# Performance work log

Hardware: AMD Instinct MI355X
Metric: run time of the kernel (lower is better)

## Reference

```python
import jax, jax.numpy as jnp
import numpy as np

B, T, N, K, IB, O = 128, 16, 65536, 8, 256, 10

def setup_inputs() -> dict:
    key = jax.random.key(0)
    ks = jax.random.split(key, 8)
    x = jax.random.randint(ks[0], (B, T, IB), 0, 2, dtype=jnp.int32)          # boolean input bits per timestep
    adj_list = jax.random.randint(ks[1], (N, K), 0, N, dtype=jnp.int32)       # incoming neighbors, homogenized
    adj_mask = jnp.ones((N, K), dtype=jnp.int32)                               # validity mask (all valid here)
    lut = jax.random.randint(ks[2], (N, 2 ** K), 0, 2, dtype=jnp.int32)        # boolean lookup table per node
    init_state = jax.random.randint(ks[3], (N,), 0, 2, dtype=jnp.int32)        # 'random' init strategy
    w_in = jnp.arange(IB, dtype=jnp.int32)                                     # input-bit -> node index map
    w_readout = jax.random.normal(ks[4], (O, N), dtype=jnp.float32) * 0.01
    b_readout = jax.random.normal(ks[5], (O,), dtype=jnp.float32)
    return dict(x=x, adj_list=adj_list, adj_mask=adj_mask, lut=lut,
                init_state=init_state, w_in=w_in,
                w_readout=w_readout, b_readout=b_readout)

def _run_reservoir(x, adj_list, adj_mask, lut, init_state, w_in):
    # x: [B,T,IB] bits; returns final boolean state [B,N] (int32)
    powers = (2 ** jnp.arange(K, dtype=jnp.int32))[::-1]   # matches powers_of_2 flip
    node_idx = jnp.arange(N, dtype=jnp.int32)
    state0 = jnp.broadcast_to(init_state[None, :], (B, N)).astype(jnp.int32)

    def step(state, xt):
        # perturb input nodes with this timestep's bits (xor perturbation)
        state = state.at[:, w_in].set(jnp.bitwise_xor(state[:, w_in], xt))
        # gather incoming-neighbor states, mask padded slots: [B,N,K]
        neigh = jnp.take(state, adj_list, axis=1) * adj_mask
        # pack K bits into LUT index, MSB-first: [B,N]
        idx = jnp.sum(neigh * powers, axis=-1)
        # per-node boolean update via LUT gather
        new_state = lut[node_idx[None, :], idx]
        return new_state, None

    xT = jnp.swapaxes(x, 0, 1)  # [T,B,IB]
    final, _ = jax.lax.scan(step, state0, xT)
    return final

def reference(x, adj_list, adj_mask, lut, init_state, w_in, w_readout, b_readout):
    final = _run_reservoir(x, adj_list, adj_mask, lut, init_state, w_in)
    logits = final.astype(jnp.float32) @ w_readout.T + b_readout  # [B,O]
    return jax.nn.sigmoid(logits)
```

## Files before the change

kernel.cpp:

```cpp
#include <hip/hip_runtime.h>
#include <stdint.h>

#define NN     65536
#define KK     8
#define BB     128
#define TT     16
#define IBITS  256
#define OO     10

#define ZIDX         (NN + IBITS)
#define SBUF_ENTRIES (NN + IBITS + 1)
#define RCHUNKS 512
#define RNODES  128

__device__ __forceinline__ uint32_t bmask(uint32_t w, int off) {
  return (uint32_t)__builtin_amdgcn_sbfe((int)w, off, 1);
}
__device__ __forceinline__ uint32_t mux(uint32_t s, uint32_t hi, uint32_t lo) {
  return ((hi ^ lo) & s) ^ lo;
}

template<int D, int BASE> struct Sh {
  static __device__ __forceinline__ void eval(const uint32_t (&L)[8],
      const uint32_t (&xa)[8], const uint32_t (&xb)[8],
      uint32_t &ra, uint32_t &rb) {
    uint32_t la, lb, ha, hb;
    Sh<D - 1, BASE>::eval(L, xa, xb, la, lb);
    Sh<D - 1, BASE + (1 << (D - 1))>::eval(L, xa, xb, ha, hb);
    ra = mux(xa[D - 1], ha, la);
    rb = mux(xb[D - 1], hb, lb);
  }
};
template<int BASE> struct Sh<2, BASE> {
  static __device__ __forceinline__ void eval(const uint32_t (&L)[8],
      const uint32_t (&xa)[8], const uint32_t (&xb)[8],
      uint32_t &ra, uint32_t &rb) {
    const uint32_t lw = L[BASE >> 5];
    const uint32_t c0 = bmask(lw, (BASE & 31) + 0);
    const uint32_t c1 = bmask(lw, (BASE & 31) + 1);
    const uint32_t c2 = bmask(lw, (BASE & 31) + 2);
    const uint32_t c3 = bmask(lw, (BASE & 31) + 3);
    uint32_t t0, t1;
    t0 = mux(xa[0], c1, c0); t1 = mux(xa[0], c3, c2); ra = mux(xa[1], t1, t0);
    t0 = mux(xb[0], c1, c0); t1 = mux(xb[0], c3, c2); rb = mux(xb[1], t1, t0);
  }
};

#define PB_LUT   2048
#define PB_MADJ  2048
#define PB_X     64
#define PB_STATE 256
#define PREP_BLOCKS (PB_LUT + PB_MADJ + PB_X + PB_STATE)

__global__ __launch_bounds__(256) void prep_kernel(
    const int* __restrict__ lut, const int* __restrict__ adj,
    const int* __restrict__ adjm, const int* __restrict__ x,
    const int* __restrict__ init,
    uint32_t* __restrict__ luttt, int* __restrict__ madj,
    uint32_t* __restrict__ xvecw, uint4* __restrict__ sA, uint4* __restrict__ sB) {
  const int b = blockIdx.x, t = threadIdx.x;
  if (b < PB_LUT) {
    const int g = b * 256 + t;
    const int n = g >> 3, w = g & 7;
    const int4* lut4 = (const int4*)lut;
    uint32_t val = 0;
#pragma unroll
    for (int q = 0; q < 8; ++q) {
      int4 v = lut4[n * 64 + w * 8 + q];
      val |= (uint32_t)(v.x & 1) << (4 * q + 0);
      val |= (uint32_t)(v.y & 1) << (4 * q + 1);
      val |= (uint32_t)(v.z & 1) << (4 * q + 2);
      val |= (uint32_t)(v.w & 1) << (4 * q + 3);
    }
    luttt[g] = val;
  } else if (b < PB_LUT + PB_MADJ) {
    const int g = (b - PB_LUT) * 256 + t;
    int a = adj[g];
    int m = adjm[g] & 1;
    madj[g] = m ? ((a < IBITS) ? a + NN : a) : ZIDX;
  } else if (b < PB_LUT + PB_MADJ + PB_X) {
    const int g = (b - PB_LUT - PB_MADJ) * 256 + t;
    const int tt = g >> 10, rest = g & 1023, i = rest >> 2, bq = rest & 3;
    uint32_t wv = 0;
#pragma unroll
    for (int bl = 0; bl < 32; ++bl) {
      int bb = bq * 32 + bl;
      wv |= (uint32_t)(x[(bb * TT + tt) * IBITS + i] & 1) << bl;
    }
    xvecw[(tt * IBITS + i) * 4 + bq] = wv;
  } else {
    const int n = (b - PB_LUT - PB_MADJ - PB_X) * 256 + t;
    uint32_t m = 0u - (uint32_t)(init[n] & 1);
    uint4 s = make_uint4(m, m, m, m);
    sA[n] = s;
    if (n < IBITS) {
      uint32_t wv[4] = {0, 0, 0, 0};
#pragma unroll
      for (int bb = 0; bb < BB; ++bb) {
        uint32_t bit = (uint32_t)(x[(bb * TT + 0) * IBITS + n] & 1);
        wv[bb >> 5] |= bit << (bb & 31);
      }
      sA[NN + n] = make_uint4(s.x ^ wv[0], s.y ^ wv[1], s.z ^ wv[2], s.w ^ wv[3]);
    }
    if (n == 0) {
      uint4 z = make_uint4(0, 0, 0, 0);
      sA[ZIDX] = z;
      sB[ZIDX] = z;
    }
  }
}

__global__ __launch_bounds__(256) void step_kernel(const uint32_t* __restrict__ sinw,
                                                   uint32_t* __restrict__ soutw,
                                                   const uint4* __restrict__ luttt,
                                                   const int* __restrict__ madj,
                                                   const uint32_t* __restrict__ xnextw) {
  const int g = blockIdx.x * 256 + threadIdx.x;
  const int n = g >> 1, h = g & 1;
  const int4* madj4 = (const int4*)madj;
  int4 a0 = madj4[n * 2 + 0], a1 = madj4[n * 2 + 1];
  uint4 l0 = luttt[n * 2 + 0], l1 = luttt[n * 2 + 1];
  const int ia[8] = {a0.x, a0.y, a0.z, a0.w, a1.x, a1.y, a1.z, a1.w};
  uint32_t xa[8], xb[8];
#pragma unroll
  for (int k = 0; k < 8; ++k) {
    uint2 gg = *(const uint2*)(sinw + (ia[k] << 2) + (h << 1));
    xa[7 - k] = gg.x;
    xb[7 - k] = gg.y;
  }
  const uint32_t L[8] = {l0.x, l0.y, l0.z, l0.w, l1.x, l1.y, l1.z, l1.w};
  uint32_t ra, rb;
  Sh<8, 0>::eval(L, xa, xb, ra, rb);
  *(uint2*)(soutw + (n << 2) + (h << 1)) = make_uint2(ra, rb);
  if (xnextw != nullptr && n < IBITS) {
    uint2 xn = *(const uint2*)(xnextw + (n << 2) + (h << 1));
    *(uint2*)(soutw + ((NN + n) << 2) + (h << 1)) = make_uint2(ra ^ xn.x, rb ^ xn.y);
  }
}

__global__ __launch_bounds__(256) void readout_kernel(const uint32_t* __restrict__ statew,
                                                      const float* __restrict__ w,
                                                      float* __restrict__ part) {
  __shared__ uint32_t sw[64 * 4];
  __shared__ float wsm[OO * 64];
  const int c = blockIdx.x;
  const int t = threadIdx.x;
  const int b = t & 127, oh = t >> 7;
  const int word = b >> 5, sh = b & 31;
  float acc[5] = {0.f, 0.f, 0.f, 0.f, 0.f};
  for (int s = 0; s < 2; ++s) {
    const int base = c * RNODES + s * 64;
    __syncthreads();
    sw[t] = statew[base * 4 + t];
#pragma unroll
    for (int r = 0; r < 3; ++r) {
      int idx = r * 256 + t;
      if (idx < OO * 64) wsm[idx] = w[(idx >> 6) * NN + base + (idx & 63)];
    }
    __syncthreads();
#pragma unroll 8
    for (int j = 0; j < 64; ++j) {
      uint32_t m = 0u - ((sw[j * 4 + word] >> sh) & 1u);
#pragma unroll
      for (int q = 0; q < 5; ++q) {
        uint32_t wv = __float_as_uint(wsm[(oh * 5 + q) * 64 + j]) & m;
        acc[q] += __uint_as_float(wv);
      }
    }
  }
#pragma unroll
  for (int q = 0; q < 5; ++q)
    part[(c * BB + b) * OO + oh * 5 + q] = acc[q];
}

__global__ __launch_bounds__(256) void finalize_kernel(const float* __restrict__ part,
                                                       const float* __restrict__ bias,
                                                       float* __restrict__ out) {
  __shared__ float red[256];
  const int i = blockIdx.x;
  const int b = i / OO, o = i % OO;
  const int t = threadIdx.x;
  float s = part[(t * BB + b) * OO + o] + part[((t + 256) * BB + b) * OO + o];
  red[t] = s;
  __syncthreads();
  for (int h = 128; h > 0; h >>= 1) {
    if (t < h) red[t] += red[t + h];
    __syncthreads();
  }
  if (t == 0) out[b * OO + o] = 1.f / (1.f + __expf(-(red[0] + bias[o])));
}

extern "C" void kernel_launch(void* const* d_in, const int* in_sizes, int n_in,
                              void* d_out, int out_size, void* d_ws, size_t ws_size,
                              hipStream_t stream) {
  const int* x    = (const int*)d_in[0];
  const int* adj  = (const int*)d_in[1];
  const int* adjm = (const int*)d_in[2];
  const int* lut  = (const int*)d_in[3];
  const int* init = (const int*)d_in[4];
  const float* wro = (const float*)d_in[6];
  const float* bro = (const float*)d_in[7];
  float* out = (float*)d_out;

  char* ws = (char*)d_ws;
  const size_t SBUF = (size_t)SBUF_ENTRIES * 16;
  uint4* sA        = (uint4*)(ws);
  uint4* sB        = (uint4*)(ws + SBUF);
  uint32_t* xvecw  = (uint32_t*)(ws + 2 * SBUF);
  uint32_t* luttt  = (uint32_t*)(ws + 2 * SBUF + (size_t)TT * IBITS * 16);
  int* madj        = (int*)(ws + 2 * SBUF + (size_t)TT * IBITS * 16 + (size_t)NN * 32);
  float* part      = (float*)(ws + 2 * SBUF + (size_t)TT * IBITS * 16 + (size_t)NN * 64);

  hipLaunchKernelGGL(prep_kernel, dim3(PREP_BLOCKS), dim3(256), 0, stream,
                     lut, adj, adjm, x, init, luttt, madj, xvecw, sA, sB);

  for (int t = 0; t < TT; ++t) {
    const uint32_t* sin = (const uint32_t*)((t & 1) ? sB : sA);
    uint32_t* sout      = (uint32_t*)((t & 1) ? sA : sB);
    const uint32_t* xn  = (t + 1 < TT) ? (xvecw + (size_t)(t + 1) * IBITS * 4) : nullptr;
    hipLaunchKernelGGL(step_kernel, dim3((NN * 2) / 256), dim3(256), 0, stream,
                       sin, sout, (const uint4*)luttt, madj, xn);
  }
  hipLaunchKernelGGL(readout_kernel, dim3(RCHUNKS), dim3(256), 0, stream,
                     (const uint32_t*)sA, wro, part);
  hipLaunchKernelGGL(finalize_kernel, dim3(BB * OO), dim3(256), 0, stream, part, bro, out);
}
```

Before: 296.0 us.

## Fuse all timesteps into one persistent kernel with a software grid barrier

Replaces the sixteen per-timestep step kernel launches with one persistent kernel of 1024 blocks. The blocks synchronize between timesteps through a striped atomic-counter grid barrier, and each thread keeps its LUT and neighbor offsets in registers across all steps. Each thread now handles one 32-batch word per node instead of two, and the counters are zeroed in the prep kernel. This removes launch gaps and the repeated reloading of LUT and adjacency data. In exchange it relies on all 1024 blocks being co-resident; otherwise the barrier deadlocks, and the barrier itself adds latency at every step.

```diff
diff --git a/kernel.cpp b/kernel.cpp
--- a/kernel.cpp
+++ b/kernel.cpp
@@ -12,6 +12,7 @@
 #define SBUF_ENTRIES (NN + IBITS + 1)
 #define RCHUNKS 512
 #define RNODES  128
+#define SP_BLOCKS 1024
 
 __device__ __forceinline__ uint32_t bmask(uint32_t w, int off) {
   return (uint32_t)__builtin_amdgcn_sbfe((int)w, off, 1);
@@ -20,29 +21,25 @@
   return ((hi ^ lo) & s) ^ lo;
 }
 
-template<int D, int BASE> struct Sh {
-  static __device__ __forceinline__ void eval(const uint32_t (&L)[8],
-      const uint32_t (&xa)[8], const uint32_t (&xb)[8],
-      uint32_t &ra, uint32_t &rb) {
-    uint32_t la, lb, ha, hb;
-    Sh<D - 1, BASE>::eval(L, xa, xb, la, lb);
-    Sh<D - 1, BASE + (1 << (D - 1))>::eval(L, xa, xb, ha, hb);
-    ra = mux(xa[D - 1], ha, la);
-    rb = mux(xb[D - 1], hb, lb);
+template<int D, int BASE> struct Sh1 {
+  static __device__ __forceinline__ uint32_t eval(const uint32_t (&L)[8],
+                                                  const uint32_t (&xv)[8]) {
+    uint32_t lo = Sh1<D - 1, BASE>::eval(L, xv);
+    uint32_t hi = Sh1<D - 1, BASE + (1 << (D - 1))>::eval(L, xv);
+    return mux(xv[D - 1], hi, lo);
   }
 };
-template<int BASE> struct Sh<2, BASE> {
-  static __device__ __forceinline__ void eval(const uint32_t (&L)[8],
-      const uint32_t (&xa)[8], const uint32_t (&xb)[8],
-      uint32_t &ra, uint32_t &rb) {
+template<int BASE> struct Sh1<2, BASE> {
+  static __device__ __forceinline__ uint32_t eval(const uint32_t (&L)[8],
+                                                  const uint32_t (&xv)[8]) {
     const uint32_t lw = L[BASE >> 5];
     const uint32_t c0 = bmask(lw, (BASE & 31) + 0);
     const uint32_t c1 = bmask(lw, (BASE & 31) + 1);
     const uint32_t c2 = bmask(lw, (BASE & 31) + 2);
     const uint32_t c3 = bmask(lw, (BASE & 31) + 3);
-    uint32_t t0, t1;
-    t0 = mux(xa[0], c1, c0); t1 = mux(xa[0], c3, c2); ra = mux(xa[1], t1, t0);
-    t0 = mux(xb[0], c1, c0); t1 = mux(xb[0], c3, c2); rb = mux(xb[1], t1, t0);
+    const uint32_t t0 = mux(xv[0], c1, c0);
+    const uint32_t t1 = mux(xv[0], c3, c2);
+    return mux(xv[1], t1, t0);
   }
 };
 
@@ -57,7 +54,8 @@
     const int* __restrict__ adjm, const int* __restrict__ x,
     const int* __restrict__ init,
     uint32_t* __restrict__ luttt, int* __restrict__ madj,
-    uint32_t* __restrict__ xvecw, uint4* __restrict__ sA, uint4* __restrict__ sB) {
+    uint32_t* __restrict__ xvecw, uint4* __restrict__ sA, uint4* __restrict__ sB,
+    uint32_t* __restrict__ ctrs) {
   const int b = blockIdx.x, t = threadIdx.x;
   if (b < PB_LUT) {
     const int g = b * 256 + t;
@@ -102,6 +100,7 @@
       }
       sA[NN + n] = make_uint4(s.x ^ wv[0], s.y ^ wv[1], s.z ^ wv[2], s.w ^ wv[3]);
     }
+    if (n < 512) ctrs[n] = 0;
     if (n == 0) {
       uint4 z = make_uint4(0, 0, 0, 0);
       sA[ZIDX] = z;
@@ -110,31 +109,58 @@
   }
 }
 
-__global__ __launch_bounds__(256) void step_kernel(const uint32_t* __restrict__ sinw,
-                                                   uint32_t* __restrict__ soutw,
-                                                   const uint4* __restrict__ luttt,
-                                                   const int* __restrict__ madj,
-                                                   const uint32_t* __restrict__ xnextw) {
+__device__ __forceinline__ void grid_barrier(uint32_t* ctrs, uint32_t phase) {
+  __syncthreads();
+  if (threadIdx.x == 0) {
+    __threadfence();
+    atomicAdd(&ctrs[(blockIdx.x & 31) * 16], 1u);
+  }
+  if (threadIdx.x < 32) {
+    const uint32_t tgt = phase * (SP_BLOCKS / 32);
+    while (__hip_atomic_load(&ctrs[threadIdx.x * 16], __ATOMIC_RELAXED,
+                             __HIP_MEMORY_SCOPE_AGENT) < tgt) {
+      __builtin_amdgcn_s_sleep(2);
+    }
+  }
+  __syncthreads();
+  if (threadIdx.x < 64) __threadfence();
+  __syncthreads();
+}
+
+__global__ __launch_bounds__(256, 4) void steps_kernel(
+    uint32_t* __restrict__ sA, uint32_t* __restrict__ sB,
+    const uint32_t* __restrict__ luttt, const int* __restrict__ madj,
+    const uint32_t* __restrict__ xvecw, uint32_t* __restrict__ ctrs) {
   const int g = blockIdx.x * 256 + threadIdx.x;
-  const int n = g >> 1, h = g & 1;
+  const int n = g >> 2, w = g & 3;
   const int4* madj4 = (const int4*)madj;
+  const uint4* lut4v = (const uint4*)luttt;
   int4 a0 = madj4[n * 2 + 0], a1 = madj4[n * 2 + 1];
-  uint4 l0 = luttt[n * 2 + 0], l1 = luttt[n * 2 + 1];
+  uint4 l0 = lut4v[n * 2 + 0], l1 = lut4v[n * 2 + 1];
+  uint32_t L[8] = {l0.x, l0.y, l0.z, l0.w, l1.x, l1.y, l1.z, l1.w};
   const int ia[8] = {a0.x, a0.y, a0.z, a0.w, a1.x, a1.y, a1.z, a1.w};
-  uint32_t xa[8], xb[8];
-#pragma unroll
-  for (int k = 0; k < 8; ++k) {
-    uint2 gg = *(const uint2*)(sinw + (ia[k] << 2) + (h << 1));
-    xa[7 - k] = gg.x;
-    xb[7 - k] = gg.y;
-  }
-  const uint32_t L[8] = {l0.x, l0.y, l0.z, l0.w, l1.x, l1.y, l1.z, l1.w};
-  uint32_t ra, rb;
-  Sh<8, 0>::eval(L, xa, xb, ra, rb);
-  *(uint2*)(soutw + (n << 2) + (h << 1)) = make_uint2(ra, rb);
-  if (xnextw != nullptr && n < IBITS) {
-    uint2 xn = *(const uint2*)(xnextw + (n << 2) + (h << 1));
-    *(uint2*)(soutw + ((NN + n) << 2) + (h << 1)) = make_uint2(ra ^ xn.x, rb ^ xn.y);
+  uint32_t off[8];
+#pragma unroll
+  for (int j = 0; j < 8; ++j) off[j] = ((uint32_t)ia[7 - j] << 4) + ((uint32_t)w << 2);
+
+  uint32_t* cur = sA;
+  uint32_t* nxt = sB;
+#pragma unroll 1
+  for (int t = 0; t < TT; ++t) {
+#pragma unroll
+    for (int i = 0; i < 8; ++i) asm volatile("" : "+v"(L[i]));
+    const char* base = (const char*)cur;
+    uint32_t xv[8];
+#pragma unroll
+    for (int j = 0; j < 8; ++j)
+      xv[j] = *(const uint32_t*)(base + off[j]);
+    uint32_t r = Sh1<8, 0>::eval(L, xv);
+    nxt[(n << 2) + w] = r;
+    if (n < IBITS && t + 1 < TT) {
+      nxt[((NN + n) << 2) + w] = r ^ xvecw[((t + 1) * IBITS + n) * 4 + w];
+    }
+    uint32_t* tmp = cur; cur = nxt; nxt = tmp;
+    if (t + 1 < TT) grid_barrier(ctrs, (uint32_t)(t + 1));
   }
 }
 
@@ -210,17 +236,15 @@
   uint32_t* luttt  = (uint32_t*)(ws + 2 * SBUF + (size_t)TT * IBITS * 16);
   int* madj        = (int*)(ws + 2 * SBUF + (size_t)TT * IBITS * 16 + (size_t)NN * 32);
   float* part      = (float*)(ws + 2 * SBUF + (size_t)TT * IBITS * 16 + (size_t)NN * 64);
+  uint32_t* ctrs   = (uint32_t*)(ws + 2 * SBUF + (size_t)TT * IBITS * 16 + (size_t)NN * 64
+                                 + (size_t)RCHUNKS * BB * OO * 4);
 
   hipLaunchKernelGGL(prep_kernel, dim3(PREP_BLOCKS), dim3(256), 0, stream,
-                     lut, adj, adjm, x, init, luttt, madj, xvecw, sA, sB);
-
-  for (int t = 0; t < TT; ++t) {
-    const uint32_t* sin = (const uint32_t*)((t & 1) ? sB : sA);
-    uint32_t* sout      = (uint32_t*)((t & 1) ? sA : sB);
-    const uint32_t* xn  = (t + 1 < TT) ? (xvecw + (size_t)(t + 1) * IBITS * 4) : nullptr;
-    hipLaunchKernelGGL(step_kernel, dim3((NN * 2) / 256), dim3(256), 0, stream,
-                       sin, sout, (const uint4*)luttt, madj, xn);
-  }
+                     lut, adj, adjm, x, init, luttt, madj, xvecw, sA, sB, ctrs);
+
+  hipLaunchKernelGGL(steps_kernel, dim3(SP_BLOCKS), dim3(256), 0, stream,
+                     (uint32_t*)sA, (uint32_t*)sB, luttt, madj, xvecw, ctrs);
+
   hipLaunchKernelGGL(readout_kernel, dim3(RCHUNKS), dim3(256), 0, stream,
                      (const uint32_t*)sA, wro, part);
   hipLaunchKernelGGL(finalize_kernel, dim3(BB * OO), dim3(256), 0, stream, part, bro, out);
```

Measured after the change: 987.1 us. 233% more time.
